# Performance work log

Hardware: AMD Instinct MI355X
Metric: run time of the kernel (lower is better)

## Reference

```python
import jax, jax.numpy as jnp
import numpy as np

USER_NUM = 60000
ITEM_NUM = 40000
NODE_NUM = USER_NUM + ITEM_NUM
EMBED_DIM = 64
N_LAYER = 3
NNZ = 1600000
BATCH = 4096
NEG_SLOPE = 0.2


def setup_inputs() -> dict:
    key = jax.random.key(0)
    ks = jax.random.split(key, 8)
    emb = jax.random.normal(ks[0], (NODE_NUM, EMBED_DIM), dtype=jnp.float32) * 0.1
    W1 = jax.random.normal(ks[1], (N_LAYER, EMBED_DIM, EMBED_DIM), dtype=jnp.float32) * 0.1
    W2 = jax.random.normal(ks[2], (N_LAYER, EMBED_DIM, EMBED_DIM), dtype=jnp.float32) * 0.1
    vals = jax.random.uniform(ks[3], (NNZ,), dtype=jnp.float32) * 0.01  # normalized Laplacian weights
    row_idx = jax.random.randint(ks[4], (NNZ,), 0, NODE_NUM, dtype=jnp.int32)
    col_idx = jax.random.randint(ks[5], (NNZ,), 0, NODE_NUM, dtype=jnp.int32)
    user_idx = jax.random.randint(ks[6], (BATCH,), 0, USER_NUM, dtype=jnp.int32)
    item_idx = jax.random.randint(ks[7], (BATCH,), 0, ITEM_NUM, dtype=jnp.int32)
    return {"emb": emb, "W1": W1, "W2": W2, "vals": vals,
            "row_idx": row_idx, "col_idx": col_idx,
            "user_idx": user_idx, "item_idx": item_idx}


def _spmm(vals, row_idx, col_idx, E):
    # L @ E with L in COO form: gather source rows, scale, scatter-add to dest rows
    msgs = vals[:, None] * E[col_idx]                       # [nnz, D]
    return jax.ops.segment_sum(msgs, row_idx, num_segments=NODE_NUM)


def reference(emb, W1, W2, vals, row_idx, col_idx, user_idx, item_idx):
    E_prev = emb
    E_list = [emb]
    for layer in range(N_LAYER):
        side_E = _spmm(vals, row_idx, col_idx, E_prev)      # [N, D]
        sum_E = side_E + E_prev
        bi_E = E_prev * side_E
        E_next = jax.nn.leaky_relu(sum_E @ W1[layer] + bi_E @ W2[layer],
                                   negative_slope=NEG_SLOPE)
        # dropout=0.0 / eval mode -> no-op
        E_prev = E_next
        E_list.append(E_next)
    E_all = jnp.concatenate(E_list, axis=1)                 # [N, D*(L+1)]
    E_user = E_all[:USER_NUM]
    E_item = E_all[USER_NUM:]
    return (E_user[user_idx], E_item[item_idx])
```

## Files before the change

### kernel.cpp

```cpp
#include <hip/hip_runtime.h>
#include <hip/hip_bf16.h>

#define USER_NUM 60000
#define ITEM_NUM 40000
#define NODE_NUM 100000
#define DIM 64
#define NNZ_N 1600000
#define BATCH 4096
#define NEG 0.2f
#define BROWS 512
#define NBKT 196
#define PA_EPT 16
#define PA_EPB (256 * PA_EPT)
#define PA_GRID ((NNZ_N + PA_EPB - 1) / PA_EPB)
#define VAL_DEC 3.0517578125e-07f
#define NTILE 6250

typedef unsigned long long u64;
typedef unsigned int u32;
typedef __attribute__((ext_vector_type(8))) short bf16x8;
typedef __attribute__((ext_vector_type(4))) float f32x4;
typedef __attribute__((ext_vector_type(2))) float f32x2;

__device__ __forceinline__ float bf2f(unsigned short u) {
    return __uint_as_float(((u32)u) << 16);
}
__device__ __forceinline__ unsigned short f2bf(float f) {
    u32 x = __float_as_uint(f);
    u32 r = (x + 0x7FFFu + ((x >> 16) & 1u)) >> 16;
    return (unsigned short)r;
}
template <bool WORD>
__device__ __forceinline__ int cvt2fp8(u32 u, int old) {
    float lo = __uint_as_float(u << 16);
    float hi = __uint_as_float(u & 0xffff0000u);
    return __builtin_amdgcn_cvt_pk_fp8_f32(lo, hi, old, WORD);
}

__global__ void k_bcount(const int* __restrict__ row, int* __restrict__ bkt_cnt,
                         const float4* __restrict__ csrc, ushort4* __restrict__ dstB,
                         u32* __restrict__ dstF, int n) {
    __shared__ int h[NBKT];
    int t = threadIdx.x;
    if (t < NBKT) h[t] = 0;
    __syncthreads();
    int base = blockIdx.x * PA_EPB;
#pragma unroll
    for (int j = 0; j < PA_EPT; j++) {
        int idx = base + j * 256 + t;
        if (idx < n) atomicAdd(&h[row[idx] >> 9], 1);
    }
    __syncthreads();
    if (t < NBKT && h[t]) atomicAdd(&bkt_cnt[t], h[t]);
    const int n4 = NODE_NUM * DIM / 4;
    for (int i = blockIdx.x * 256 + t; i < n4; i += PA_GRID * 256) {
        float4 f = csrc[i];
        dstB[i] = make_ushort4(f2bf(f.x), f2bf(f.y), f2bf(f.z), f2bf(f.w));
        int w = __builtin_amdgcn_cvt_pk_fp8_f32(f.x, f.y, 0, false);
        w = __builtin_amdgcn_cvt_pk_fp8_f32(f.z, f.w, w, true);
        dstF[i] = (u32)w;
    }
}

__launch_bounds__(256)
__global__ void k_passA(const int* __restrict__ row, const int* __restrict__ col,
                        const float* __restrict__ vals, const int* __restrict__ bkt_cnt,
                        int* __restrict__ bcur0, u64* __restrict__ tpk, int n) {
    __shared__ int sb[256];
    __shared__ int gbase[NBKT];
    __shared__ int cur[NBKT];
    __shared__ int gb[NBKT];
    int t = threadIdx.x;
    sb[t] = (t < NBKT) ? bkt_cnt[t] : 0;
    if (t < NBKT) cur[t] = 0;
    __syncthreads();
    for (int d = 1; d < 256; d <<= 1) {
        int x = (t >= d) ? sb[t - d] : 0;
        __syncthreads();
        sb[t] += x;
        __syncthreads();
    }
    if (t < NBKT) gbase[t] = sb[t] - bkt_cnt[t];
    __syncthreads();
    int base = blockIdx.x * PA_EPB;
    u64 pk[PA_EPT];
    int rk[PA_EPT], bk[PA_EPT];
#pragma unroll
    for (int j = 0; j < PA_EPT; j++) {
        int idx = base + j * 256 + t;
        if (idx < n) {
            int r = row[idx];
            int c = col[idx];
            int bits = (int)rintf(vals[idx] * 3276800.0f);
            if (bits > 32767) bits = 32767;
            pk[j] = ((u64)(u32)r << 32) | ((u32)c << 15) | (u32)bits;
            bk[j] = r >> 9;
            rk[j] = atomicAdd(&cur[bk[j]], 1);
        } else bk[j] = -1;
    }
    __syncthreads();
    if (t < NBKT) {
        int cnt = cur[t];
        gb[t] = gbase[t] + (cnt ? atomicAdd(&bcur0[t], cnt) : 0);
    }
    __syncthreads();
#pragma unroll
    for (int j = 0; j < PA_EPT; j++) {
        if (bk[j] >= 0) tpk[gb[bk[j]] + rk[j]] = pk[j];
    }
}

__launch_bounds__(512)
__global__ void k_passB(const u64* __restrict__ tpk, const int* __restrict__ bkt_cnt,
                        int* __restrict__ ptr, u32* __restrict__ ecv,
                        int* __restrict__ rord) {
    __shared__ int sh[512];
    __shared__ int sb[256];
    __shared__ int h2[64];
    __shared__ int h2c[64];
    int b = blockIdx.x, t = threadIdx.x;
    if (t < 256) sb[t] = (t < NBKT) ? bkt_cnt[t] : 0;
    if (t < 64) { h2[t] = 0; h2c[t] = 0; }
    sh[t] = 0;
    __syncthreads();
    for (int d = 1; d < 256; d <<= 1) {
        int x = 0;
        if (t < 256 && t >= d) x = sb[t - d];
        __syncthreads();
        if (t < 256) sb[t] += x;
        __syncthreads();
    }
    int start = sb[b] - bkt_cnt[b];
    int end = sb[b];
    for (int i = start + t; i < end; i += 512)
        atomicAdd(&sh[(int)(tpk[i] >> 32) & 511], 1);
    __syncthreads();
    int cnt = sh[t];
    int rowg = (b << 9) + t;
    bool valid = (rowg < NODE_NUM);
    int bin = cnt > 63 ? 63 : cnt;
    if (valid) atomicAdd(&h2[bin], 1);
    for (int d = 1; d < 512; d <<= 1) {
        int x = (t >= d) ? sh[t - d] : 0;
        __syncthreads();
        sh[t] += x;
        __syncthreads();
    }
    int excl = sh[t] - cnt;
    if (valid) ptr[rowg] = start + excl;
    if (b == NBKT - 1 && t == 0) ptr[NODE_NUM] = NNZ_N;
    __syncthreads();
    sh[t] = excl;
    __syncthreads();
    for (int i = start + t; i < end; i += 512) {
        u64 e = tpk[i];
        int r = (int)(e >> 32);
        int pos = start + atomicAdd(&sh[r & 511], 1);
        ecv[pos] = (u32)e;
    }
    __syncthreads();
    if (t < 64) sb[t] = h2[t];
    __syncthreads();
    for (int d = 1; d < 64; d <<= 1) {
        int x = 0;
        if (t < 64 && t >= d) x = sb[t - d];
        __syncthreads();
        if (t < 64) sb[t] += x;
        __syncthreads();
    }
    if (valid) {
        int h2base = sb[bin] - h2[bin];
        int rank = atomicAdd(&h2c[bin], 1);
        rord[(b << 9) + h2base + rank] = rowg;
    }
}

__launch_bounds__(256)
__global__ void k_spmm(const int* __restrict__ ptrS, const int* __restrict__ rord,
                       const u32* __restrict__ ecv, const unsigned char* __restrict__ Ef,
                       unsigned short* __restrict__ S) {
    int wave = (blockIdx.x * 256 + threadIdx.x) >> 6;
    int lane = threadIdx.x & 63;
    int L = lane & 7;
    int rslot = wave * 8 + (lane >> 3);
    int myrow = rord[rslot];
    int s = ptrS[myrow];
    int e = ptrS[myrow + 1];
    int dm = e - s;
    dm = max(dm, __shfl_xor(dm, 8));
    dm = max(dm, __shfl_xor(dm, 16));
    dm = max(dm, __shfl_xor(dm, 32));
    float acc[8];
#pragma unroll
    for (int q = 0; q < 8; q++) acc[q] = 0.f;
    int srcbase = lane & 56;
    for (int off = 0; off < dm; off += 8) {
        int idx = s + off + L;
        u32 u = (idx < e) ? ecv[idx] : 0u;
#pragma unroll
        for (int j = 0; j < 8; j++) {
            u32 uu = __shfl(u, srcbase | j);
            float fv = (float)(uu & 0x7fffu);
            uint2 gw = *(const uint2*)&Ef[(size_t)(uu >> 15) * 64 + L * 8];
            f32x2 g01 = __builtin_amdgcn_cvt_pk_f32_fp8(gw.x, false);
            f32x2 g23 = __builtin_amdgcn_cvt_pk_f32_fp8(gw.x, true);
            f32x2 g45 = __builtin_amdgcn_cvt_pk_f32_fp8(gw.y, false);
            f32x2 g67 = __builtin_amdgcn_cvt_pk_f32_fp8(gw.y, true);
            acc[0] = fmaf(fv, g01.x, acc[0]);
            acc[1] = fmaf(fv, g01.y, acc[1]);
            acc[2] = fmaf(fv, g23.x, acc[2]);
            acc[3] = fmaf(fv, g23.y, acc[3]);
            acc[4] = fmaf(fv, g45.x, acc[4]);
            acc[5] = fmaf(fv, g45.y, acc[5]);
            acc[6] = fmaf(fv, g67.x, acc[6]);
            acc[7] = fmaf(fv, g67.y, acc[7]);
        }
    }
    u32 o[4];
#pragma unroll
    for (int q = 0; q < 4; q++) {
        float x0 = acc[2 * q] * VAL_DEC;
        float x1 = acc[2 * q + 1] * VAL_DEC;
        o[q] = (u32)f2bf(x0) | ((u32)f2bf(x1) << 16);
    }
    *(uint4*)&S[(size_t)myrow * 64 + L * 8] = make_uint4(o[0], o[1], o[2], o[3]);
}

__launch_bounds__(256)
__global__ void k_dmm(const unsigned short* __restrict__ Ein,
                      const unsigned short* __restrict__ S,
                      const float* __restrict__ W1l, const float* __restrict__ W2l,
                      unsigned short* __restrict__ Eout, unsigned char* __restrict__ Eout8) {
    __shared__ unsigned short cbuf[4][16 * 68];
    int t = threadIdx.x;
    int w = t >> 6;
    int lane = t & 63;
    int r16 = lane & 15;
    int g = lane >> 4;

    bf16x8 bw[2][2][4];
#pragma unroll
    for (int mat = 0; mat < 2; mat++) {
        const float* W = mat ? W2l : W1l;
#pragma unroll
        for (int kc = 0; kc < 2; kc++) {
#pragma unroll
            for (int cb = 0; cb < 4; cb++) {
                int col = cb * 16 + r16;
                int k0 = kc * 32 + g * 8;
                bf16x8 f;
#pragma unroll
                for (int j = 0; j < 8; j++)
                    f[j] = (short)f2bf(W[(k0 + j) * 64 + col]);
                bw[mat][kc][cb] = f;
            }
        }
    }

    for (int tile = blockIdx.x * 4 + w; tile < NTILE; tile += gridDim.x * 4) {
        int row0 = tile * 16;
        const unsigned short* ep = &Ein[(size_t)(row0 + r16) * 64 + g * 8];
        const unsigned short* sp = &S[(size_t)(row0 + r16) * 64 + g * 8];
        f32x4 ac0 = {0.f, 0.f, 0.f, 0.f};
        f32x4 ac1 = {0.f, 0.f, 0.f, 0.f};
        f32x4 ac2 = {0.f, 0.f, 0.f, 0.f};
        f32x4 ac3 = {0.f, 0.f, 0.f, 0.f};
#pragma unroll
        for (int kc = 0; kc < 2; kc++) {
            bf16x8 ev = *(const bf16x8*)(ep + kc * 32);
            bf16x8 sv = *(const bf16x8*)(sp + kc * 32);
            bf16x8 su, bi;
#pragma unroll
            for (int j = 0; j < 8; j++) {
                float e = bf2f((unsigned short)ev[j]);
                float s = bf2f((unsigned short)sv[j]);
                su[j] = (short)f2bf(e + s);
                bi[j] = (short)f2bf(e * s);
            }
            ac0 = __builtin_amdgcn_mfma_f32_16x16x32_bf16(su, bw[0][kc][0], ac0, 0, 0, 0);
            ac0 = __builtin_amdgcn_mfma_f32_16x16x32_bf16(bi, bw[1][kc][0], ac0, 0, 0, 0);
            ac1 = __builtin_amdgcn_mfma_f32_16x16x32_bf16(su, bw[0][kc][1], ac1, 0, 0, 0);
            ac1 = __builtin_amdgcn_mfma_f32_16x16x32_bf16(bi, bw[1][kc][1], ac1, 0, 0, 0);
            ac2 = __builtin_amdgcn_mfma_f32_16x16x32_bf16(su, bw[0][kc][2], ac2, 0, 0, 0);
            ac2 = __builtin_amdgcn_mfma_f32_16x16x32_bf16(bi, bw[1][kc][2], ac2, 0, 0, 0);
            ac3 = __builtin_amdgcn_mfma_f32_16x16x32_bf16(su, bw[0][kc][3], ac3, 0, 0, 0);
            ac3 = __builtin_amdgcn_mfma_f32_16x16x32_bf16(bi, bw[1][kc][3], ac3, 0, 0, 0);
        }
#pragma unroll
        for (int reg = 0; reg < 4; reg++) {
            int crow = g * 4 + reg;
            float x0 = ac0[reg]; x0 = x0 > 0.f ? x0 : NEG * x0;
            float x1 = ac1[reg]; x1 = x1 > 0.f ? x1 : NEG * x1;
            float x2 = ac2[reg]; x2 = x2 > 0.f ? x2 : NEG * x2;
            float x3 = ac3[reg]; x3 = x3 > 0.f ? x3 : NEG * x3;
            cbuf[w][crow * 68 + 0 * 16 + r16] = f2bf(x0);
            cbuf[w][crow * 68 + 1 * 16 + r16] = f2bf(x1);
            cbuf[w][crow * 68 + 2 * 16 + r16] = f2bf(x2);
            cbuf[w][crow * 68 + 3 * 16 + r16] = f2bf(x3);
        }
        int rrow = lane >> 2;
        int q = lane & 3;
        const uint4* lp = (const uint4*)&cbuf[w][rrow * 68 + q * 16];
        uint4 v0 = lp[0];
        uint4 v1 = lp[1];
        uint4* gp = (uint4*)&Eout[(size_t)(row0 + rrow) * 64 + q * 16];
        gp[0] = v0;
        gp[1] = v1;
        if (Eout8 != nullptr) {
            int w0 = cvt2fp8<false>(v0.x, 0); w0 = cvt2fp8<true>(v0.y, w0);
            int w1 = cvt2fp8<false>(v0.z, 0); w1 = cvt2fp8<true>(v0.w, w1);
            int w2 = cvt2fp8<false>(v1.x, 0); w2 = cvt2fp8<true>(v1.y, w2);
            int w3 = cvt2fp8<false>(v1.z, 0); w3 = cvt2fp8<true>(v1.w, w3);
            *(uint4*)&Eout8[(size_t)(row0 + rrow) * 64 + q * 16] =
                make_uint4((u32)w0, (u32)w1, (u32)w2, (u32)w3);
        }
    }
}

__global__ void k_gatherAll(const float* __restrict__ emb,
                            const unsigned short* __restrict__ E1,
                            const unsigned short* __restrict__ E2,
                            const unsigned short* __restrict__ E3,
                            float* __restrict__ out,
                            const int* __restrict__ uidx, const int* __restrict__ iidx) {
    int g = blockIdx.x * 256 + threadIdx.x;
    int b = g >> 6, d = g & 63;
    if (b >= 2 * BATCH) return;
    int node;
    size_t obase;
    if (b < BATCH) { node = uidx[b]; obase = (size_t)b * 256; }
    else { int bb = b - BATCH; node = USER_NUM + iidx[bb]; obase = (size_t)BATCH * 256 + (size_t)bb * 256; }
    size_t nb = (size_t)node * 64 + d;
    out[obase + d]       = emb[nb];
    out[obase + 64 + d]  = bf2f(E1[nb]);
    out[obase + 128 + d] = bf2f(E2[nb]);
    out[obase + 192 + d] = bf2f(E3[nb]);
}

extern "C" void kernel_launch(void* const* d_in, const int* in_sizes, int n_in,
                              void* d_out, int out_size, void* d_ws, size_t ws_size,
                              hipStream_t stream) {
    const float* emb  = (const float*)d_in[0];
    const float* W1   = (const float*)d_in[1];
    const float* W2   = (const float*)d_in[2];
    const float* vals = (const float*)d_in[3];
    const int*   row  = (const int*)d_in[4];
    const int*   col  = (const int*)d_in[5];
    const int*   uidx = (const int*)d_in[6];
    const int*   iidx = (const int*)d_in[7];
    float* out = (float*)d_out;

    char* p = (char*)d_ws;
    auto alloc = [&](size_t bytes) -> void* {
        void* q = (void*)p;
        p += (bytes + 255) & ~(size_t)255;
        return q;
    };
    int*            ptr      = (int*)alloc((size_t)(NODE_NUM + 1) * 4);
    int*            bcnt_cur = (int*)alloc(512 * 4);
    int*            rord     = (int*)alloc((size_t)NODE_NUM * 4);
    u32*            ecv      = (u32*)alloc((size_t)NNZ_N * 4);
    u64*            tpk      = (u64*)alloc((size_t)NNZ_N * 8);
    unsigned short* Sb       = (unsigned short*)alloc((size_t)NODE_NUM * DIM * 2);
    unsigned short* Ebf0     = (unsigned short*)alloc((size_t)NODE_NUM * DIM * 2);
    unsigned short* Eba      = (unsigned short*)alloc((size_t)NODE_NUM * DIM * 2);
    unsigned short* Ebb      = (unsigned short*)alloc((size_t)NODE_NUM * DIM * 2);
    unsigned char*  Ef0      = (unsigned char*)alloc((size_t)NODE_NUM * DIM);
    unsigned char*  Efa      = (unsigned char*)alloc((size_t)NODE_NUM * DIM);
    unsigned char*  Efb      = (unsigned char*)alloc((size_t)NODE_NUM * DIM);
    int* bkt_cnt = bcnt_cur;
    int* bcur0   = bcnt_cur + 256;
    unsigned short* Ebc = (unsigned short*)tpk;

    hipMemsetAsync(bcnt_cur, 0, 512 * 4, stream);
    k_bcount<<<PA_GRID, 256, 0, stream>>>(row, bkt_cnt, (const float4*)emb,
                                          (ushort4*)Ebf0, (u32*)Ef0, NNZ_N);
    k_passA<<<PA_GRID, 256, 0, stream>>>(row, col, vals, bkt_cnt, bcur0, tpk, NNZ_N);
    k_passB<<<NBKT, 512, 0, stream>>>(tpk, bkt_cnt, ptr, ecv, rord);

    const int SPMM_GRID = NODE_NUM / 32;
    const int DMM_GRID = 391;
    k_spmm<<<SPMM_GRID, 256, 0, stream>>>(ptr, rord, ecv, Ef0, Sb);
    k_dmm<<<DMM_GRID, 256, 0, stream>>>(Ebf0, Sb, W1, W2, Eba, Efa);

    k_spmm<<<SPMM_GRID, 256, 0, stream>>>(ptr, rord, ecv, Efa, Sb);
    k_dmm<<<DMM_GRID, 256, 0, stream>>>(Eba, Sb, W1 + 4096, W2 + 4096, Ebc, Efb);

    k_spmm<<<SPMM_GRID, 256, 0, stream>>>(ptr, rord, ecv, Efb, Sb);
    k_dmm<<<DMM_GRID, 256, 0, stream>>>(Ebc, Sb, W1 + 8192, W2 + 8192, Ebb, (unsigned char*)nullptr);

    k_gatherAll<<<2048, 256, 0, stream>>>(emb, Eba, Ebc, Ebb, out, uidx, iidx);
}
```

Measured before the change: 192.3 us.

## Fuse CSR build passes into one cooperative kernel with grid syncs

Merges the memset, bucket count, bucket scatter and per-bucket sort kernels into a single cooperative launch that uses grid-wide syncs between phases. Buckets shrink from 512 to 256 rows, so there are 391 buckets, matching the 391-block grid, and each block sorts one bucket with 256 threads. The aim is to remove launch gaps and the memset, at the cost of grid-sync overhead and one block per bucket doing the later phase with fewer threads.

```diff
diff --git a/kernel.cpp b/kernel.cpp
--- a/kernel.cpp
+++ b/kernel.cpp
@@ -1,5 +1,8 @@
 #include <hip/hip_runtime.h>
 #include <hip/hip_bf16.h>
+#include <hip/hip_cooperative_groups.h>
+
+namespace cg = cooperative_groups;
 
 #define USER_NUM 60000
 #define ITEM_NUM 40000
@@ -8,11 +11,11 @@
 #define NNZ_N 1600000
 #define BATCH 4096
 #define NEG 0.2f
-#define BROWS 512
-#define NBKT 196
+#define BROWS 256
+#define NBKT 391
 #define PA_EPT 16
 #define PA_EPB (256 * PA_EPT)
-#define PA_GRID ((NNZ_N + PA_EPB - 1) / PA_EPB)
+#define BGRID 391
 #define VAL_DEC 3.0517578125e-07f
 #define NTILE 6250
 
@@ -37,141 +40,143 @@
     return __builtin_amdgcn_cvt_pk_fp8_f32(lo, hi, old, WORD);
 }
 
-__global__ void k_bcount(const int* __restrict__ row, int* __restrict__ bkt_cnt,
-                         const float4* __restrict__ csrc, ushort4* __restrict__ dstB,
-                         u32* __restrict__ dstF, int n) {
-    __shared__ int h[NBKT];
+__global__ void k_build(const int* __restrict__ row, const int* __restrict__ col,
+                        const float* __restrict__ vals, int* __restrict__ bkt_cnt,
+                        int* __restrict__ bcur0, int* __restrict__ gba,
+                        u64* __restrict__ tpk, int* __restrict__ ptr,
+                        u32* __restrict__ ecv, int* __restrict__ rord,
+                        const float4* __restrict__ csrc, ushort4* __restrict__ dstB,
+                        u32* __restrict__ dstF) {
+    __shared__ int s_h[NBKT];
+    __shared__ int s_g[NBKT];
+    __shared__ int s_b[NBKT];
+    __shared__ int s_ps[256];
+    __shared__ int s_sh[256];
+    __shared__ int s_h2[64];
+    __shared__ int s_h2c[64];
+    cg::grid_group grid = cg::this_grid();
     int t = threadIdx.x;
-    if (t < NBKT) h[t] = 0;
-    __syncthreads();
-    int base = blockIdx.x * PA_EPB;
+    int blk = blockIdx.x;
+
+    if (blk == 0) {
+        for (int i = t; i < NBKT; i += 256) { bkt_cnt[i] = 0; bcur0[i] = 0; }
+    }
+    grid.sync();
+
+    for (int i = t; i < NBKT; i += 256) s_h[i] = 0;
+    __syncthreads();
+    int base = blk * PA_EPB;
 #pragma unroll
     for (int j = 0; j < PA_EPT; j++) {
         int idx = base + j * 256 + t;
-        if (idx < n) atomicAdd(&h[row[idx] >> 9], 1);
-    }
-    __syncthreads();
-    if (t < NBKT && h[t]) atomicAdd(&bkt_cnt[t], h[t]);
+        if (idx < NNZ_N) atomicAdd(&s_h[row[idx] >> 8], 1);
+    }
+    __syncthreads();
+    for (int i = t; i < NBKT; i += 256)
+        if (s_h[i]) atomicAdd(&bkt_cnt[i], s_h[i]);
     const int n4 = NODE_NUM * DIM / 4;
-    for (int i = blockIdx.x * 256 + t; i < n4; i += PA_GRID * 256) {
+    for (int i = blk * 256 + t; i < n4; i += BGRID * 256) {
         float4 f = csrc[i];
         dstB[i] = make_ushort4(f2bf(f.x), f2bf(f.y), f2bf(f.z), f2bf(f.w));
         int w = __builtin_amdgcn_cvt_pk_fp8_f32(f.x, f.y, 0, false);
         w = __builtin_amdgcn_cvt_pk_fp8_f32(f.z, f.w, w, true);
         dstF[i] = (u32)w;
     }
-}
-
-__launch_bounds__(256)
-__global__ void k_passA(const int* __restrict__ row, const int* __restrict__ col,
-                        const float* __restrict__ vals, const int* __restrict__ bkt_cnt,
-                        int* __restrict__ bcur0, u64* __restrict__ tpk, int n) {
-    __shared__ int sb[256];
-    __shared__ int gbase[NBKT];
-    __shared__ int cur[NBKT];
-    __shared__ int gb[NBKT];
-    int t = threadIdx.x;
-    sb[t] = (t < NBKT) ? bkt_cnt[t] : 0;
-    if (t < NBKT) cur[t] = 0;
-    __syncthreads();
-    for (int d = 1; d < 256; d <<= 1) {
-        int x = (t >= d) ? sb[t - d] : 0;
-        __syncthreads();
-        sb[t] += x;
-        __syncthreads();
-    }
-    if (t < NBKT) gbase[t] = sb[t] - bkt_cnt[t];
-    __syncthreads();
-    int base = blockIdx.x * PA_EPB;
-    u64 pk[PA_EPT];
-    int rk[PA_EPT], bk[PA_EPT];
-#pragma unroll
-    for (int j = 0; j < PA_EPT; j++) {
-        int idx = base + j * 256 + t;
-        if (idx < n) {
-            int r = row[idx];
-            int c = col[idx];
-            int bits = (int)rintf(vals[idx] * 3276800.0f);
-            if (bits > 32767) bits = 32767;
-            pk[j] = ((u64)(u32)r << 32) | ((u32)c << 15) | (u32)bits;
-            bk[j] = r >> 9;
-            rk[j] = atomicAdd(&cur[bk[j]], 1);
-        } else bk[j] = -1;
-    }
-    __syncthreads();
-    if (t < NBKT) {
-        int cnt = cur[t];
-        gb[t] = gbase[t] + (cnt ? atomicAdd(&bcur0[t], cnt) : 0);
-    }
-    __syncthreads();
-#pragma unroll
-    for (int j = 0; j < PA_EPT; j++) {
-        if (bk[j] >= 0) tpk[gb[bk[j]] + rk[j]] = pk[j];
-    }
-}
-
-__launch_bounds__(512)
-__global__ void k_passB(const u64* __restrict__ tpk, const int* __restrict__ bkt_cnt,
-                        int* __restrict__ ptr, u32* __restrict__ ecv,
-                        int* __restrict__ rord) {
-    __shared__ int sh[512];
-    __shared__ int sb[256];
-    __shared__ int h2[64];
-    __shared__ int h2c[64];
-    int b = blockIdx.x, t = threadIdx.x;
-    if (t < 256) sb[t] = (t < NBKT) ? bkt_cnt[t] : 0;
-    if (t < 64) { h2[t] = 0; h2c[t] = 0; }
-    sh[t] = 0;
-    __syncthreads();
-    for (int d = 1; d < 256; d <<= 1) {
-        int x = 0;
-        if (t < 256 && t >= d) x = sb[t - d];
-        __syncthreads();
-        if (t < 256) sb[t] += x;
-        __syncthreads();
-    }
-    int start = sb[b] - bkt_cnt[b];
-    int end = sb[b];
-    for (int i = start + t; i < end; i += 512)
-        atomicAdd(&sh[(int)(tpk[i] >> 32) & 511], 1);
-    __syncthreads();
-    int cnt = sh[t];
-    int rowg = (b << 9) + t;
+    grid.sync();
+
+    {
+        int c0 = (2 * t < NBKT) ? bkt_cnt[2 * t] : 0;
+        int c1 = (2 * t + 1 < NBKT) ? bkt_cnt[2 * t + 1] : 0;
+        s_ps[t] = c0 + c1;
+        for (int i = t; i < NBKT; i += 256) s_h[i] = 0;
+        __syncthreads();
+        for (int d = 1; d < 256; d <<= 1) {
+            int x = (t >= d) ? s_ps[t - d] : 0;
+            __syncthreads();
+            s_ps[t] += x;
+            __syncthreads();
+        }
+        int pexcl = (t > 0) ? s_ps[t - 1] : 0;
+        if (2 * t < NBKT) s_g[2 * t] = pexcl;
+        if (2 * t + 1 < NBKT) s_g[2 * t + 1] = pexcl + c0;
+        __syncthreads();
+        if (blk == 0) {
+            for (int i = t; i < NBKT; i += 256) gba[i] = s_g[i];
+        }
+        u64 pk[PA_EPT];
+        int rk[PA_EPT], bk[PA_EPT];
+#pragma unroll
+        for (int j = 0; j < PA_EPT; j++) {
+            int idx = base + j * 256 + t;
+            if (idx < NNZ_N) {
+                int r = row[idx];
+                int c = col[idx];
+                int bits = (int)rintf(vals[idx] * 3276800.0f);
+                if (bits > 32767) bits = 32767;
+                pk[j] = ((u64)(u32)r << 32) | ((u32)c << 15) | (u32)bits;
+                bk[j] = r >> 8;
+                rk[j] = atomicAdd(&s_h[bk[j]], 1);
+            } else bk[j] = -1;
+        }
+        __syncthreads();
+        for (int i = t; i < NBKT; i += 256) {
+            int cnt = s_h[i];
+            s_b[i] = s_g[i] + (cnt ? atomicAdd(&bcur0[i], cnt) : 0);
+        }
+        __syncthreads();
+#pragma unroll
+        for (int j = 0; j < PA_EPT; j++) {
+            if (bk[j] >= 0) tpk[s_b[bk[j]] + rk[j]] = pk[j];
+        }
+    }
+    grid.sync();
+
+    if (blk >= NBKT) return;
+    int start = gba[blk];
+    int end = start + bkt_cnt[blk];
+    s_sh[t] = 0;
+    if (t < 64) { s_h2[t] = 0; s_h2c[t] = 0; }
+    __syncthreads();
+    for (int i = start + t; i < end; i += 256)
+        atomicAdd(&s_sh[(int)(tpk[i] >> 32) & 255], 1);
+    __syncthreads();
+    int cnt = s_sh[t];
+    int rowg = (blk << 8) + t;
     bool valid = (rowg < NODE_NUM);
     int bin = cnt > 63 ? 63 : cnt;
-    if (valid) atomicAdd(&h2[bin], 1);
-    for (int d = 1; d < 512; d <<= 1) {
-        int x = (t >= d) ? sh[t - d] : 0;
-        __syncthreads();
-        sh[t] += x;
-        __syncthreads();
-    }
-    int excl = sh[t] - cnt;
+    if (valid) atomicAdd(&s_h2[bin], 1);
+    for (int d = 1; d < 256; d <<= 1) {
+        int x = (t >= d) ? s_sh[t - d] : 0;
+        __syncthreads();
+        s_sh[t] += x;
+        __syncthreads();
+    }
+    int excl = s_sh[t] - cnt;
     if (valid) ptr[rowg] = start + excl;
-    if (b == NBKT - 1 && t == 0) ptr[NODE_NUM] = NNZ_N;
-    __syncthreads();
-    sh[t] = excl;
-    __syncthreads();
-    for (int i = start + t; i < end; i += 512) {
+    if (blk == NBKT - 1 && t == 0) ptr[NODE_NUM] = NNZ_N;
+    __syncthreads();
+    s_sh[t] = excl;
+    __syncthreads();
+    for (int i = start + t; i < end; i += 256) {
         u64 e = tpk[i];
         int r = (int)(e >> 32);
-        int pos = start + atomicAdd(&sh[r & 511], 1);
+        int pos = start + atomicAdd(&s_sh[r & 255], 1);
         ecv[pos] = (u32)e;
     }
     __syncthreads();
-    if (t < 64) sb[t] = h2[t];
+    if (t < 64) s_ps[t] = s_h2[t];
     __syncthreads();
     for (int d = 1; d < 64; d <<= 1) {
         int x = 0;
-        if (t < 64 && t >= d) x = sb[t - d];
-        __syncthreads();
-        if (t < 64) sb[t] += x;
+        if (t < 64 && t >= d) x = s_ps[t - d];
+        __syncthreads();
+        if (t < 64) s_ps[t] += x;
         __syncthreads();
     }
     if (valid) {
-        int h2base = sb[bin] - h2[bin];
-        int rank = atomicAdd(&h2c[bin], 1);
-        rord[(b << 9) + h2base + rank] = rowg;
+        int h2base = s_ps[bin] - s_h2[bin];
+        int rank = atomicAdd(&s_h2c[bin], 1);
+        rord[(blk << 8) + h2base + rank] = rowg;
     }
 }
 
@@ -340,14 +345,14 @@
 extern "C" void kernel_launch(void* const* d_in, const int* in_sizes, int n_in,
                               void* d_out, int out_size, void* d_ws, size_t ws_size,
                               hipStream_t stream) {
+    const int*   row  = (const int*)d_in[4];
+    const int*   col  = (const int*)d_in[5];
+    const int*   uidx = (const int*)d_in[6];
+    const int*   iidx = (const int*)d_in[7];
     const float* emb  = (const float*)d_in[0];
     const float* W1   = (const float*)d_in[1];
     const float* W2   = (const float*)d_in[2];
     const float* vals = (const float*)d_in[3];
-    const int*   row  = (const int*)d_in[4];
-    const int*   col  = (const int*)d_in[5];
-    const int*   uidx = (const int*)d_in[6];
-    const int*   iidx = (const int*)d_in[7];
     float* out = (float*)d_out;
 
     char* p = (char*)d_ws;
@@ -357,7 +362,9 @@
         return q;
     };
     int*            ptr      = (int*)alloc((size_t)(NODE_NUM + 1) * 4);
-    int*            bcnt_cur = (int*)alloc(512 * 4);
+    int*            bkt_cnt  = (int*)alloc(NBKT * 4);
+    int*            bcur0    = (int*)alloc(NBKT * 4);
+    int*            gba      = (int*)alloc(NBKT * 4);
     int*            rord     = (int*)alloc((size_t)NODE_NUM * 4);
     u32*            ecv      = (u32*)alloc((size_t)NNZ_N * 4);
     u64*            tpk      = (u64*)alloc((size_t)NNZ_N * 8);
@@ -368,15 +375,18 @@
     unsigned char*  Ef0      = (unsigned char*)alloc((size_t)NODE_NUM * DIM);
     unsigned char*  Efa      = (unsigned char*)alloc((size_t)NODE_NUM * DIM);
     unsigned char*  Efb      = (unsigned char*)alloc((size_t)NODE_NUM * DIM);
-    int* bkt_cnt = bcnt_cur;
-    int* bcur0   = bcnt_cur + 256;
     unsigned short* Ebc = (unsigned short*)tpk;
 
-    hipMemsetAsync(bcnt_cur, 0, 512 * 4, stream);
-    k_bcount<<<PA_GRID, 256, 0, stream>>>(row, bkt_cnt, (const float4*)emb,
-                                          (ushort4*)Ebf0, (u32*)Ef0, NNZ_N);
-    k_passA<<<PA_GRID, 256, 0, stream>>>(row, col, vals, bkt_cnt, bcur0, tpk, NNZ_N);
-    k_passB<<<NBKT, 512, 0, stream>>>(tpk, bkt_cnt, ptr, ecv, rord);
+    {
+        const float4* csrc = (const float4*)emb;
+        ushort4* dstB = (ushort4*)Ebf0;
+        u32* dstF = (u32*)Ef0;
+        void* args[] = {(void*)&row, (void*)&col, (void*)&vals, (void*)&bkt_cnt,
+                        (void*)&bcur0, (void*)&gba, (void*)&tpk, (void*)&ptr,
+                        (void*)&ecv, (void*)&rord, (void*)&csrc, (void*)&dstB,
+                        (void*)&dstF};
+        hipLaunchCooperativeKernel((void*)k_build, dim3(BGRID), dim3(256), args, 0, stream);
+    }
 
     const int SPMM_GRID = NODE_NUM / 32;
     const int DMM_GRID = 391;
```

Measured after the change: 335.6 us. 1.74x slower.

## Fuse SpMM and dense layer transform into one per-layer kernel via LDS

Applied to the files above, without the earlier changes.

Merges the sparse aggregation and the MFMA-based dense transform into a single kernel per layer. Each wave now aggregates 16 rows, with 4 lanes per row and 16 features per lane, and stages the bf16 result in shared memory. The MFMA stage reads it from there, so the global S buffer and its write and read round trip go away, along with three launches. The cost is that every wave reloads and converts the W matrices for only one tile. Rows are processed in rord order, so E loads and stores become scattered, and the wider per-lane loads change gather efficiency and register pressure.

```diff
diff --git a/kernel.cpp b/kernel.cpp
--- a/kernel.cpp
+++ b/kernel.cpp
@@ -176,68 +176,74 @@
 }
 
 __launch_bounds__(256)
-__global__ void k_spmm(const int* __restrict__ ptrS, const int* __restrict__ rord,
-                       const u32* __restrict__ ecv, const unsigned char* __restrict__ Ef,
-                       unsigned short* __restrict__ S) {
-    int wave = (blockIdx.x * 256 + threadIdx.x) >> 6;
-    int lane = threadIdx.x & 63;
-    int L = lane & 7;
-    int rslot = wave * 8 + (lane >> 3);
-    int myrow = rord[rslot];
-    int s = ptrS[myrow];
-    int e = ptrS[myrow + 1];
-    int dm = e - s;
-    dm = max(dm, __shfl_xor(dm, 8));
-    dm = max(dm, __shfl_xor(dm, 16));
-    dm = max(dm, __shfl_xor(dm, 32));
-    float acc[8];
-#pragma unroll
-    for (int q = 0; q < 8; q++) acc[q] = 0.f;
-    int srcbase = lane & 56;
-    for (int off = 0; off < dm; off += 8) {
-        int idx = s + off + L;
-        u32 u = (idx < e) ? ecv[idx] : 0u;
-#pragma unroll
-        for (int j = 0; j < 8; j++) {
-            u32 uu = __shfl(u, srcbase | j);
-            float fv = (float)(uu & 0x7fffu);
-            uint2 gw = *(const uint2*)&Ef[(size_t)(uu >> 15) * 64 + L * 8];
-            f32x2 g01 = __builtin_amdgcn_cvt_pk_f32_fp8(gw.x, false);
-            f32x2 g23 = __builtin_amdgcn_cvt_pk_f32_fp8(gw.x, true);
-            f32x2 g45 = __builtin_amdgcn_cvt_pk_f32_fp8(gw.y, false);
-            f32x2 g67 = __builtin_amdgcn_cvt_pk_f32_fp8(gw.y, true);
-            acc[0] = fmaf(fv, g01.x, acc[0]);
-            acc[1] = fmaf(fv, g01.y, acc[1]);
-            acc[2] = fmaf(fv, g23.x, acc[2]);
-            acc[3] = fmaf(fv, g23.y, acc[3]);
-            acc[4] = fmaf(fv, g45.x, acc[4]);
-            acc[5] = fmaf(fv, g45.y, acc[5]);
-            acc[6] = fmaf(fv, g67.x, acc[6]);
-            acc[7] = fmaf(fv, g67.y, acc[7]);
-        }
-    }
-    u32 o[4];
-#pragma unroll
-    for (int q = 0; q < 4; q++) {
-        float x0 = acc[2 * q] * VAL_DEC;
-        float x1 = acc[2 * q + 1] * VAL_DEC;
-        o[q] = (u32)f2bf(x0) | ((u32)f2bf(x1) << 16);
-    }
-    *(uint4*)&S[(size_t)myrow * 64 + L * 8] = make_uint4(o[0], o[1], o[2], o[3]);
-}
-
-__launch_bounds__(256)
-__global__ void k_dmm(const unsigned short* __restrict__ Ein,
-                      const unsigned short* __restrict__ S,
-                      const float* __restrict__ W1l, const float* __restrict__ W2l,
-                      unsigned short* __restrict__ Eout, unsigned char* __restrict__ Eout8) {
+__global__ void k_layer(const int* __restrict__ ptrS, const int* __restrict__ rord,
+                        const u32* __restrict__ ecv, const unsigned char* __restrict__ Ef,
+                        const unsigned short* __restrict__ Ein,
+                        const float* __restrict__ W1l, const float* __restrict__ W2l,
+                        unsigned short* __restrict__ Eout, unsigned char* __restrict__ Eout8) {
+    __shared__ unsigned short sS[4][16 * 64];
     __shared__ unsigned short cbuf[4][16 * 68];
     int t = threadIdx.x;
     int w = t >> 6;
     int lane = t & 63;
+    int tile = blockIdx.x * 4 + w;
+    if (tile >= NTILE) return;
+
+    int rowL = lane >> 2;
+    int q4 = lane & 3;
+    int arow = rord[tile * 16 + rowL];
+    int s0 = ptrS[arow];
+    int e0 = ptrS[arow + 1];
+    int dm = e0 - s0;
+    dm = max(dm, __shfl_xor(dm, 4));
+    dm = max(dm, __shfl_xor(dm, 8));
+    dm = max(dm, __shfl_xor(dm, 16));
+    dm = max(dm, __shfl_xor(dm, 32));
+    float acc[16];
+#pragma unroll
+    for (int q = 0; q < 16; q++) acc[q] = 0.f;
+    int srcbase = lane & 60;
+    for (int off = 0; off < dm; off += 4) {
+        int idx = s0 + off + q4;
+        u32 u = (idx < e0) ? ecv[idx] : 0u;
+#pragma unroll
+        for (int j = 0; j < 4; j++) {
+            u32 uu = __shfl(u, srcbase | j);
+            float fv = (float)(uu & 0x7fffu);
+            uint4 gw = *(const uint4*)&Ef[(size_t)(uu >> 15) * 64 + q4 * 16];
+            f32x2 ga = __builtin_amdgcn_cvt_pk_f32_fp8(gw.x, false);
+            f32x2 gb = __builtin_amdgcn_cvt_pk_f32_fp8(gw.x, true);
+            f32x2 gc = __builtin_amdgcn_cvt_pk_f32_fp8(gw.y, false);
+            f32x2 gd = __builtin_amdgcn_cvt_pk_f32_fp8(gw.y, true);
+            f32x2 ge = __builtin_amdgcn_cvt_pk_f32_fp8(gw.z, false);
+            f32x2 gf = __builtin_amdgcn_cvt_pk_f32_fp8(gw.z, true);
+            f32x2 gg = __builtin_amdgcn_cvt_pk_f32_fp8(gw.w, false);
+            f32x2 gh = __builtin_amdgcn_cvt_pk_f32_fp8(gw.w, true);
+            acc[0]  = fmaf(fv, ga.x, acc[0]);  acc[1]  = fmaf(fv, ga.y, acc[1]);
+            acc[2]  = fmaf(fv, gb.x, acc[2]);  acc[3]  = fmaf(fv, gb.y, acc[3]);
+            acc[4]  = fmaf(fv, gc.x, acc[4]);  acc[5]  = fmaf(fv, gc.y, acc[5]);
+            acc[6]  = fmaf(fv, gd.x, acc[6]);  acc[7]  = fmaf(fv, gd.y, acc[7]);
+            acc[8]  = fmaf(fv, ge.x, acc[8]);  acc[9]  = fmaf(fv, ge.y, acc[9]);
+            acc[10] = fmaf(fv, gf.x, acc[10]); acc[11] = fmaf(fv, gf.y, acc[11]);
+            acc[12] = fmaf(fv, gg.x, acc[12]); acc[13] = fmaf(fv, gg.y, acc[13]);
+            acc[14] = fmaf(fv, gh.x, acc[14]); acc[15] = fmaf(fv, gh.y, acc[15]);
+        }
+    }
+    {
+        u32 so[8];
+#pragma unroll
+        for (int q = 0; q < 8; q++) {
+            float x0 = acc[2 * q] * VAL_DEC;
+            float x1 = acc[2 * q + 1] * VAL_DEC;
+            so[q] = (u32)f2bf(x0) | ((u32)f2bf(x1) << 16);
+        }
+        uint4* sp0 = (uint4*)&sS[w][rowL * 64 + q4 * 16];
+        sp0[0] = make_uint4(so[0], so[1], so[2], so[3]);
+        sp0[1] = make_uint4(so[4], so[5], so[6], so[7]);
+    }
+
     int r16 = lane & 15;
     int g = lane >> 4;
-
     bf16x8 bw[2][2][4];
 #pragma unroll
     for (int mat = 0; mat < 2; mat++) {
@@ -256,64 +262,62 @@
             }
         }
     }
-
-    for (int tile = blockIdx.x * 4 + w; tile < NTILE; tile += gridDim.x * 4) {
-        int row0 = tile * 16;
-        const unsigned short* ep = &Ein[(size_t)(row0 + r16) * 64 + g * 8];
-        const unsigned short* sp = &S[(size_t)(row0 + r16) * 64 + g * 8];
-        f32x4 ac0 = {0.f, 0.f, 0.f, 0.f};
-        f32x4 ac1 = {0.f, 0.f, 0.f, 0.f};
-        f32x4 ac2 = {0.f, 0.f, 0.f, 0.f};
-        f32x4 ac3 = {0.f, 0.f, 0.f, 0.f};
-#pragma unroll
-        for (int kc = 0; kc < 2; kc++) {
-            bf16x8 ev = *(const bf16x8*)(ep + kc * 32);
-            bf16x8 sv = *(const bf16x8*)(sp + kc * 32);
-            bf16x8 su, bi;
-#pragma unroll
-            for (int j = 0; j < 8; j++) {
-                float e = bf2f((unsigned short)ev[j]);
-                float s = bf2f((unsigned short)sv[j]);
-                su[j] = (short)f2bf(e + s);
-                bi[j] = (short)f2bf(e * s);
-            }
-            ac0 = __builtin_amdgcn_mfma_f32_16x16x32_bf16(su, bw[0][kc][0], ac0, 0, 0, 0);
-            ac0 = __builtin_amdgcn_mfma_f32_16x16x32_bf16(bi, bw[1][kc][0], ac0, 0, 0, 0);
-            ac1 = __builtin_amdgcn_mfma_f32_16x16x32_bf16(su, bw[0][kc][1], ac1, 0, 0, 0);
-            ac1 = __builtin_amdgcn_mfma_f32_16x16x32_bf16(bi, bw[1][kc][1], ac1, 0, 0, 0);
-            ac2 = __builtin_amdgcn_mfma_f32_16x16x32_bf16(su, bw[0][kc][2], ac2, 0, 0, 0);
-            ac2 = __builtin_amdgcn_mfma_f32_16x16x32_bf16(bi, bw[1][kc][2], ac2, 0, 0, 0);
-            ac3 = __builtin_amdgcn_mfma_f32_16x16x32_bf16(su, bw[0][kc][3], ac3, 0, 0, 0);
-            ac3 = __builtin_amdgcn_mfma_f32_16x16x32_bf16(bi, bw[1][kc][3], ac3, 0, 0, 0);
+    int mrow = rord[tile * 16 + r16];
+    const unsigned short* ep = &Ein[(size_t)mrow * 64 + g * 8];
+    const unsigned short* sp = &sS[w][r16 * 64 + g * 8];
+    f32x4 ac0 = {0.f, 0.f, 0.f, 0.f};
+    f32x4 ac1 = {0.f, 0.f, 0.f, 0.f};
+    f32x4 ac2 = {0.f, 0.f, 0.f, 0.f};
+    f32x4 ac3 = {0.f, 0.f, 0.f, 0.f};
+#pragma unroll
+    for (int kc = 0; kc < 2; kc++) {
+        bf16x8 ev = *(const bf16x8*)(ep + kc * 32);
+        bf16x8 sv = *(const bf16x8*)(sp + kc * 32);
+        bf16x8 su, bi;
+#pragma unroll
+        for (int j = 0; j < 8; j++) {
+            float e = bf2f((unsigned short)ev[j]);
+            float s = bf2f((unsigned short)sv[j]);
+            su[j] = (short)f2bf(e + s);
+            bi[j] = (short)f2bf(e * s);
         }
-#pragma unroll
-        for (int reg = 0; reg < 4; reg++) {
-            int crow = g * 4 + reg;
-            float x0 = ac0[reg]; x0 = x0 > 0.f ? x0 : NEG * x0;
-            float x1 = ac1[reg]; x1 = x1 > 0.f ? x1 : NEG * x1;
-            float x2 = ac2[reg]; x2 = x2 > 0.f ? x2 : NEG * x2;
-            float x3 = ac3[reg]; x3 = x3 > 0.f ? x3 : NEG * x3;
-            cbuf[w][crow * 68 + 0 * 16 + r16] = f2bf(x0);
-            cbuf[w][crow * 68 + 1 * 16 + r16] = f2bf(x1);
-            cbuf[w][crow * 68 + 2 * 16 + r16] = f2bf(x2);
-            cbuf[w][crow * 68 + 3 * 16 + r16] = f2bf(x3);
-        }
-        int rrow = lane >> 2;
-        int q = lane & 3;
-        const uint4* lp = (const uint4*)&cbuf[w][rrow * 68 + q * 16];
-        uint4 v0 = lp[0];
-        uint4 v1 = lp[1];
-        uint4* gp = (uint4*)&Eout[(size_t)(row0 + rrow) * 64 + q * 16];
-        gp[0] = v0;
-        gp[1] = v1;
-        if (Eout8 != nullptr) {
-            int w0 = cvt2fp8<false>(v0.x, 0); w0 = cvt2fp8<true>(v0.y, w0);
-            int w1 = cvt2fp8<false>(v0.z, 0); w1 = cvt2fp8<true>(v0.w, w1);
-            int w2 = cvt2fp8<false>(v1.x, 0); w2 = cvt2fp8<true>(v1.y, w2);
-            int w3 = cvt2fp8<false>(v1.z, 0); w3 = cvt2fp8<true>(v1.w, w3);
-            *(uint4*)&Eout8[(size_t)(row0 + rrow) * 64 + q * 16] =
-                make_uint4((u32)w0, (u32)w1, (u32)w2, (u32)w3);
-        }
+        ac0 = __builtin_amdgcn_mfma_f32_16x16x32_bf16(su, bw[0][kc][0], ac0, 0, 0, 0);
+        ac0 = __builtin_amdgcn_mfma_f32_16x16x32_bf16(bi, bw[1][kc][0], ac0, 0, 0, 0);
+        ac1 = __builtin_amdgcn_mfma_f32_16x16x32_bf16(su, bw[0][kc][1], ac1, 0, 0, 0);
+        ac1 = __builtin_amdgcn_mfma_f32_16x16x32_bf16(bi, bw[1][kc][1], ac1, 0, 0, 0);
+        ac2 = __builtin_amdgcn_mfma_f32_16x16x32_bf16(su, bw[0][kc][2], ac2, 0, 0, 0);
+        ac2 = __builtin_amdgcn_mfma_f32_16x16x32_bf16(bi, bw[1][kc][2], ac2, 0, 0, 0);
+        ac3 = __builtin_amdgcn_mfma_f32_16x16x32_bf16(su, bw[0][kc][3], ac3, 0, 0, 0);
+        ac3 = __builtin_amdgcn_mfma_f32_16x16x32_bf16(bi, bw[1][kc][3], ac3, 0, 0, 0);
+    }
+#pragma unroll
+    for (int reg = 0; reg < 4; reg++) {
+        int crow = g * 4 + reg;
+        float x0 = ac0[reg]; x0 = x0 > 0.f ? x0 : NEG * x0;
+        float x1 = ac1[reg]; x1 = x1 > 0.f ? x1 : NEG * x1;
+        float x2 = ac2[reg]; x2 = x2 > 0.f ? x2 : NEG * x2;
+        float x3 = ac3[reg]; x3 = x3 > 0.f ? x3 : NEG * x3;
+        cbuf[w][crow * 68 + 0 * 16 + r16] = f2bf(x0);
+        cbuf[w][crow * 68 + 1 * 16 + r16] = f2bf(x1);
+        cbuf[w][crow * 68 + 2 * 16 + r16] = f2bf(x2);
+        cbuf[w][crow * 68 + 3 * 16 + r16] = f2bf(x3);
+    }
+    int rrow = lane >> 2;
+    int q = lane & 3;
+    int orow = rord[tile * 16 + rrow];
+    const uint4* lp = (const uint4*)&cbuf[w][rrow * 68 + q * 16];
+    uint4 v0 = lp[0];
+    uint4 v1 = lp[1];
+    uint4* gp = (uint4*)&Eout[(size_t)orow * 64 + q * 16];
+    gp[0] = v0;
+    gp[1] = v1;
+    if (Eout8 != nullptr) {
+        int w0 = cvt2fp8<false>(v0.x, 0); w0 = cvt2fp8<true>(v0.y, w0);
+        int w1 = cvt2fp8<false>(v0.z, 0); w1 = cvt2fp8<true>(v0.w, w1);
+        int w2 = cvt2fp8<false>(v1.x, 0); w2 = cvt2fp8<true>(v1.y, w2);
+        int w3 = cvt2fp8<false>(v1.z, 0); w3 = cvt2fp8<true>(v1.w, w3);
+        *(uint4*)&Eout8[(size_t)orow * 64 + q * 16] =
+            make_uint4((u32)w0, (u32)w1, (u32)w2, (u32)w3);
     }
 }
 
@@ -361,7 +365,6 @@
     int*            rord     = (int*)alloc((size_t)NODE_NUM * 4);
     u32*            ecv      = (u32*)alloc((size_t)NNZ_N * 4);
     u64*            tpk      = (u64*)alloc((size_t)NNZ_N * 8);
-    unsigned short* Sb       = (unsigned short*)alloc((size_t)NODE_NUM * DIM * 2);
     unsigned short* Ebf0     = (unsigned short*)alloc((size_t)NODE_NUM * DIM * 2);
     unsigned short* Eba      = (unsigned short*)alloc((size_t)NODE_NUM * DIM * 2);
     unsigned short* Ebb      = (unsigned short*)alloc((size_t)NODE_NUM * DIM * 2);
@@ -378,16 +381,11 @@
     k_passA<<<PA_GRID, 256, 0, stream>>>(row, col, vals, bkt_cnt, bcur0, tpk, NNZ_N);
     k_passB<<<NBKT, 512, 0, stream>>>(tpk, bkt_cnt, ptr, ecv, rord);
 
-    const int SPMM_GRID = NODE_NUM / 32;
-    const int DMM_GRID = 391;
-    k_spmm<<<SPMM_GRID, 256, 0, stream>>>(ptr, rord, ecv, Ef0, Sb);
-    k_dmm<<<DMM_GRID, 256, 0, stream>>>(Ebf0, Sb, W1, W2, Eba, Efa);
-
-    k_spmm<<<SPMM_GRID, 256, 0, stream>>>(ptr, rord, ecv, Efa, Sb);
-    k_dmm<<<DMM_GRID, 256, 0, stream>>>(Eba, Sb, W1 + 4096, W2 + 4096, Ebc, Efb);
-
-    k_spmm<<<SPMM_GRID, 256, 0, stream>>>(ptr, rord, ecv, Efb, Sb);
-    k_dmm<<<DMM_GRID, 256, 0, stream>>>(Ebc, Sb, W1 + 8192, W2 + 8192, Ebb, (unsigned char*)nullptr);
+    const int LGRID = (NTILE + 3) / 4;
+    k_layer<<<LGRID, 256, 0, stream>>>(ptr, rord, ecv, Ef0, Ebf0, W1, W2, Eba, Efa);
+    k_layer<<<LGRID, 256, 0, stream>>>(ptr, rord, ecv, Efa, Eba, W1 + 4096, W2 + 4096, Ebc, Efb);
+    k_layer<<<LGRID, 256, 0, stream>>>(ptr, rord, ecv, Efb, Ebc, W1 + 8192, W2 + 8192, Ebb,
+                                       (unsigned char*)nullptr);
 
     k_gatherAll<<<2048, 256, 0, stream>>>(emb, Eba, Ebc, Ebb, out, uidx, iidx);
 }
```

Result: no change. 192.1 us (-0.1%).

## Slice FP8 embedding table into four 16-column planes for cache-local SpMM

Applied to the files above, without the earlier changes.

The FP8 embedding copy is stored as four column slices of 16 bytes per node, each slice a contiguous 1.6MB plane, and the SpMM kernel processes one slice per block. Consecutive blocks cover the four slices of each 16-row tile, so each gather touches a smaller working set that is more likely to stay in L2/LLC. The cost is that the edge index stream is read four times (with nontemporal loads) and there are four times as many, narrower gathers. Tiles are also processed in reverse rord order.

```diff
diff --git a/kernel.cpp b/kernel.cpp
--- a/kernel.cpp
+++ b/kernel.cpp
@@ -15,6 +15,7 @@
 #define PA_GRID ((NNZ_N + PA_EPB - 1) / PA_EPB)
 #define VAL_DEC 3.0517578125e-07f
 #define NTILE 6250
+#define SLB ((size_t)NODE_NUM * 16)
 
 typedef unsigned long long u64;
 typedef unsigned int u32;
@@ -39,7 +40,7 @@
 
 __global__ void k_bcount(const int* __restrict__ row, int* __restrict__ bkt_cnt,
                          const float4* __restrict__ csrc, ushort4* __restrict__ dstB,
-                         u32* __restrict__ dstF, int n) {
+                         unsigned char* __restrict__ dstF8, int n) {
     __shared__ int h[NBKT];
     int t = threadIdx.x;
     if (t < NBKT) h[t] = 0;
@@ -58,7 +59,10 @@
         dstB[i] = make_ushort4(f2bf(f.x), f2bf(f.y), f2bf(f.z), f2bf(f.w));
         int w = __builtin_amdgcn_cvt_pk_fp8_f32(f.x, f.y, 0, false);
         w = __builtin_amdgcn_cvt_pk_fp8_f32(f.z, f.w, w, true);
-        dstF[i] = (u32)w;
+        int r = i >> 4;
+        int q = (i >> 2) & 3;
+        int o = i & 3;
+        *(u32*)&dstF8[(size_t)q * SLB + (size_t)r * 16 + o * 4] = (u32)w;
     }
 }
 
@@ -177,53 +181,47 @@
 
 __launch_bounds__(256)
 __global__ void k_spmm(const int* __restrict__ ptrS, const int* __restrict__ rord,
-                       const u32* __restrict__ ecv, const unsigned char* __restrict__ Ef,
+                       const u32* __restrict__ ecv, const unsigned char* __restrict__ Efs,
                        unsigned short* __restrict__ S) {
-    int wave = (blockIdx.x * 256 + threadIdx.x) >> 6;
-    int lane = threadIdx.x & 63;
-    int L = lane & 7;
-    int rslot = wave * 8 + (lane >> 3);
-    int myrow = rord[rslot];
-    int s = ptrS[myrow];
-    int e = ptrS[myrow + 1];
-    int dm = e - s;
+    int t = threadIdx.x;
+    int w = t >> 6;
+    int lane = t & 63;
+    int slice = blockIdx.x & 3;
+    int tile_rank = (blockIdx.x >> 2) * 4 + w;
+    if (tile_rank >= NTILE) return;
+    int tile = (NTILE - 1) - tile_rank;
+    int rowL = lane >> 2;
+    int d4 = lane & 3;
+    int r = rord[tile * 16 + rowL];
+    int s0 = ptrS[r];
+    int e0 = ptrS[r + 1];
+    int dm = e0 - s0;
+    dm = max(dm, __shfl_xor(dm, 4));
     dm = max(dm, __shfl_xor(dm, 8));
     dm = max(dm, __shfl_xor(dm, 16));
     dm = max(dm, __shfl_xor(dm, 32));
-    float acc[8];
-#pragma unroll
-    for (int q = 0; q < 8; q++) acc[q] = 0.f;
-    int srcbase = lane & 56;
-    for (int off = 0; off < dm; off += 8) {
-        int idx = s + off + L;
-        u32 u = (idx < e) ? ecv[idx] : 0u;
-#pragma unroll
-        for (int j = 0; j < 8; j++) {
+    float a0 = 0.f, a1 = 0.f, a2 = 0.f, a3 = 0.f;
+    const unsigned char* T = Efs + (size_t)slice * SLB;
+    int srcbase = lane & 60;
+    for (int off = 0; off < dm; off += 4) {
+        int idx = s0 + off + d4;
+        u32 u = (idx < e0) ? __builtin_nontemporal_load(&ecv[idx]) : 0u;
+#pragma unroll
+        for (int j = 0; j < 4; j++) {
             u32 uu = __shfl(u, srcbase | j);
             float fv = (float)(uu & 0x7fffu);
-            uint2 gw = *(const uint2*)&Ef[(size_t)(uu >> 15) * 64 + L * 8];
-            f32x2 g01 = __builtin_amdgcn_cvt_pk_f32_fp8(gw.x, false);
-            f32x2 g23 = __builtin_amdgcn_cvt_pk_f32_fp8(gw.x, true);
-            f32x2 g45 = __builtin_amdgcn_cvt_pk_f32_fp8(gw.y, false);
-            f32x2 g67 = __builtin_amdgcn_cvt_pk_f32_fp8(gw.y, true);
-            acc[0] = fmaf(fv, g01.x, acc[0]);
-            acc[1] = fmaf(fv, g01.y, acc[1]);
-            acc[2] = fmaf(fv, g23.x, acc[2]);
-            acc[3] = fmaf(fv, g23.y, acc[3]);
-            acc[4] = fmaf(fv, g45.x, acc[4]);
-            acc[5] = fmaf(fv, g45.y, acc[5]);
-            acc[6] = fmaf(fv, g67.x, acc[6]);
-            acc[7] = fmaf(fv, g67.y, acc[7]);
-        }
-    }
-    u32 o[4];
-#pragma unroll
-    for (int q = 0; q < 4; q++) {
-        float x0 = acc[2 * q] * VAL_DEC;
-        float x1 = acc[2 * q + 1] * VAL_DEC;
-        o[q] = (u32)f2bf(x0) | ((u32)f2bf(x1) << 16);
-    }
-    *(uint4*)&S[(size_t)myrow * 64 + L * 8] = make_uint4(o[0], o[1], o[2], o[3]);
+            u32 g = *(const u32*)&T[(size_t)(uu >> 15) * 16 + d4 * 4];
+            f32x2 g01 = __builtin_amdgcn_cvt_pk_f32_fp8(g, false);
+            f32x2 g23 = __builtin_amdgcn_cvt_pk_f32_fp8(g, true);
+            a0 = fmaf(fv, g01.x, a0);
+            a1 = fmaf(fv, g01.y, a1);
+            a2 = fmaf(fv, g23.x, a2);
+            a3 = fmaf(fv, g23.y, a3);
+        }
+    }
+    u32 o0 = (u32)f2bf(a0 * VAL_DEC) | ((u32)f2bf(a1 * VAL_DEC) << 16);
+    u32 o1 = (u32)f2bf(a2 * VAL_DEC) | ((u32)f2bf(a3 * VAL_DEC) << 16);
+    *(uint2*)&S[(size_t)r * 64 + slice * 16 + d4 * 4] = make_uint2(o0, o1);
 }
 
 __launch_bounds__(256)
@@ -311,7 +309,7 @@
             int w1 = cvt2fp8<false>(v0.z, 0); w1 = cvt2fp8<true>(v0.w, w1);
             int w2 = cvt2fp8<false>(v1.x, 0); w2 = cvt2fp8<true>(v1.y, w2);
             int w3 = cvt2fp8<false>(v1.z, 0); w3 = cvt2fp8<true>(v1.w, w3);
-            *(uint4*)&Eout8[(size_t)(row0 + rrow) * 64 + q * 16] =
+            *(uint4*)&Eout8[(size_t)q * SLB + (size_t)(row0 + rrow) * 16] =
                 make_uint4((u32)w0, (u32)w1, (u32)w2, (u32)w3);
         }
     }
@@ -374,11 +372,11 @@
 
     hipMemsetAsync(bcnt_cur, 0, 512 * 4, stream);
     k_bcount<<<PA_GRID, 256, 0, stream>>>(row, bkt_cnt, (const float4*)emb,
-                                          (ushort4*)Ebf0, (u32*)Ef0, NNZ_N);
+                                          (ushort4*)Ebf0, Ef0, NNZ_N);
     k_passA<<<PA_GRID, 256, 0, stream>>>(row, col, vals, bkt_cnt, bcur0, tpk, NNZ_N);
     k_passB<<<NBKT, 512, 0, stream>>>(tpk, bkt_cnt, ptr, ecv, rord);
 
-    const int SPMM_GRID = NODE_NUM / 32;
+    const int SPMM_GRID = 4 * 1563;
     const int DMM_GRID = 391;
     k_spmm<<<SPMM_GRID, 256, 0, stream>>>(ptr, rord, ecv, Ef0, Sb);
     k_dmm<<<DMM_GRID, 256, 0, stream>>>(Ebf0, Sb, W1, W2, Eba, Efa);
@@ -387,7 +385,8 @@
     k_dmm<<<DMM_GRID, 256, 0, stream>>>(Eba, Sb, W1 + 4096, W2 + 4096, Ebc, Efb);
 
     k_spmm<<<SPMM_GRID, 256, 0, stream>>>(ptr, rord, ecv, Efb, Sb);
-    k_dmm<<<DMM_GRID, 256, 0, stream>>>(Ebc, Sb, W1 + 8192, W2 + 8192, Ebb, (unsigned char*)nullptr);
+    k_dmm<<<DMM_GRID, 256, 0, stream>>>(Ebc, Sb, W1 + 8192, W2 + 8192, Ebb,
+                                        (unsigned char*)nullptr);
 
     k_gatherAll<<<2048, 256, 0, stream>>>(emb, Eba, Ebc, Ebb, out, uidx, iidx);
 }
```

New measurement: 385.6 us. 2x slower.
